# Optimization experiments

Hardware: AMD Instinct MI355X
Metric: run time of the kernel (lower is better)

The kernel has to match this reference:

```python
import jax, jax.numpy as jnp
import numpy as np

HEADS = 8
DIM_HEAD = 64
SCALE = DIM_HEAD ** -0.5


def setup_inputs() -> dict:
    key = jax.random.key(0)
    ks = jax.random.split(key, 5)
    B, N, D = 2, 4096, 512
    x = jax.random.normal(ks[0], (B, N, D), dtype=jnp.float32)
    Wq = jax.random.normal(ks[1], (D, D), dtype=jnp.float32) * (D ** -0.5)
    Wk = jax.random.normal(ks[2], (D, D), dtype=jnp.float32) * (D ** -0.5)
    Wv = jax.random.normal(ks[3], (D, D), dtype=jnp.float32) * (D ** -0.5)
    Wo = jax.random.normal(ks[4], (D, D), dtype=jnp.float32) * (D ** -0.5)
    bo = jnp.zeros((D,), dtype=jnp.float32)
    return {"x": x, "Wq": Wq, "Wk": Wk, "Wv": Wv, "Wo": Wo, "bo": bo}


def reference(x, Wq, Wk, Wv, Wo, bo):
    B, N, D = x.shape
    h, d = HEADS, DIM_HEAD
    # torch nn.Linear: y = x @ W.T
    q = (x @ Wq.T).reshape(B, N, h, d).transpose(0, 2, 1, 3)  # b h n d
    k = (x @ Wk.T).reshape(B, N, h, d).transpose(0, 2, 1, 3)
    v = (x @ Wv.T).reshape(B, N, h, d).transpose(0, 2, 1, 3)
    # fp32 score path (ATTN_PRECISION='fp32')
    sim = jnp.einsum('bhid,bhjd->bhij', q.astype(jnp.float32), k.astype(jnp.float32)) * SCALE
    attn = jax.nn.softmax(sim, axis=-1).astype(v.dtype)
    out = jnp.einsum('bhij,bhjd->bhid', attn, v)  # b h n d
    out = out.transpose(0, 2, 1, 3).reshape(B, N, h * d)  # b n (h d)
    return out @ Wo.T + bo
```

## Files before the change

kernel.cpp:

```cpp
#include <hip/hip_runtime.h>
#include <hip/hip_bf16.h>

#define B_ 2
#define N_ 4096
#define D_ 512
#define H_ 8
#define M_ (B_*N_)
#define QSCALE_ 0.18033688011f

typedef short bf16x8 __attribute__((ext_vector_type(8)));
typedef float f32x4  __attribute__((ext_vector_type(4)));

static __device__ __forceinline__ unsigned short f2bf(float f) {
    union { float f; unsigned int u; } v; v.f = f;
    unsigned int r = v.u + 0x7fffu + ((v.u >> 16) & 1u);
    return (unsigned short)(r >> 16);
}
static __device__ __forceinline__ float bf2f(unsigned short h) {
    union { unsigned int u; float f; } v; v.u = ((unsigned int)h) << 16;
    return v.f;
}
static __device__ __forceinline__ unsigned int cvt_pk_bf16(float a, float b) {
    unsigned int r;
    asm("v_cvt_pk_bf16_f32 %0, %1, %2" : "=v"(r) : "v"(a), "v"(b));
    return r;
}

__global__ void conv_all(const float* __restrict__ x,
                         const float* __restrict__ w0, const float* __restrict__ w1,
                         const float* __restrict__ w2, const float* __restrict__ w3,
                         unsigned short* __restrict__ xh, unsigned short* __restrict__ xl,
                         unsigned short* __restrict__ wh, unsigned short* __restrict__ wl)
{
    const int i = blockIdx.x * 256 + threadIdx.x;
    float4 v;
    ushort4* dh;
    ushort4* dl;
    if (i < 1048576) {
        v = ((const float4*)x)[i];
        dh = (ushort4*)xh + i;
        dl = (ushort4*)xl + i;
    } else {
        const int j = i - 1048576;
        const int w = j >> 16, di = j & 65535;
        const float* src = w == 0 ? w0 : w == 1 ? w1 : w == 2 ? w2 : w3;
        v = ((const float4*)src)[di];
        dh = (ushort4*)(wh + (size_t)w * 262144) + di;
        dl = (ushort4*)(wl + (size_t)w * 262144) + di;
    }
    ushort4 hv, lv;
    hv.x = f2bf(v.x); hv.y = f2bf(v.y); hv.z = f2bf(v.z); hv.w = f2bf(v.w);
    lv.x = f2bf(v.x - bf2f(hv.x)); lv.y = f2bf(v.y - bf2f(hv.y));
    lv.z = f2bf(v.z - bf2f(hv.z)); lv.w = f2bf(v.w - bf2f(hv.w));
    *dh = hv;
    *dl = lv;
}

template<int MODE>
__global__ __launch_bounds__(256, 2) void gemm_mfma(
    const unsigned short* __restrict__ Ah, const unsigned short* __restrict__ Al,
    const unsigned short* __restrict__ Wh, const unsigned short* __restrict__ Wl,
    const float* __restrict__ bias, float* __restrict__ outF,
    unsigned short* __restrict__ oh0, unsigned short* __restrict__ ol0,
    unsigned short* __restrict__ oh1, unsigned short* __restrict__ ol1,
    unsigned short* __restrict__ oh2, unsigned short* __restrict__ ol2,
    float scale0)
{
    __shared__ unsigned short At[2][8192];
    __shared__ unsigned short Bt[2][8192];

    const int t = threadIdx.x;
    const int lane = t & 63, wave = t >> 6;
    const int l15 = lane & 15, g = lane >> 4;
    const int wr = wave >> 1, wc = wave & 1;
    const int mb = blockIdx.x * 128;

    int which = 0, nbeff;
    if (MODE == 1) { which = blockIdx.y >> 2; nbeff = (blockIdx.y & 3) * 128; }
    else           { nbeff = blockIdx.y * 128; }
    const unsigned short* Whp = Wh + (size_t)which * 262144;
    const unsigned short* Wlp = Wl + (size_t)which * 262144;

    const int srow = t >> 1, sh = t & 1;
    const size_t gAr = (size_t)(mb + srow) * 512 + sh * 16;
    const size_t gBr = (size_t)(nbeff + srow) * 512 + sh * 16;
    const int sw = srow & 7;
    const int dA0 = srow * 64 + (((sh * 2 + 0) ^ sw) * 8);
    const int dA1 = srow * 64 + (((sh * 2 + 1) ^ sw) * 8);
    const int dA2 = srow * 64 + (((sh * 2 + 4) ^ sw) * 8);
    const int dA3 = srow * 64 + (((sh * 2 + 5) ^ sw) * 8);

    bf16x8 sA[4], sB[4];
#define GLOAD(K0) do {                                                              \
        sA[0] = *(const bf16x8*)&Ah[gAr + (K0)];  sA[1] = *(const bf16x8*)&Ah[gAr + (K0) + 8];  \
        sA[2] = *(const bf16x8*)&Al[gAr + (K0)];  sA[3] = *(const bf16x8*)&Al[gAr + (K0) + 8];  \
        sB[0] = *(const bf16x8*)&Whp[gBr + (K0)]; sB[1] = *(const bf16x8*)&Whp[gBr + (K0) + 8]; \
        sB[2] = *(const bf16x8*)&Wlp[gBr + (K0)]; sB[3] = *(const bf16x8*)&Wlp[gBr + (K0) + 8]; \
    } while (0)
#define SWRITE(BB) do {                                                             \
        *(bf16x8*)&At[BB][dA0] = sA[0]; *(bf16x8*)&At[BB][dA1] = sA[1];             \
        *(bf16x8*)&At[BB][dA2] = sA[2]; *(bf16x8*)&At[BB][dA3] = sA[3];             \
        *(bf16x8*)&Bt[BB][dA0] = sB[0]; *(bf16x8*)&Bt[BB][dA1] = sB[1];             \
        *(bf16x8*)&Bt[BB][dA2] = sB[2]; *(bf16x8*)&Bt[BB][dA3] = sB[3];             \
    } while (0)

    f32x4 acc[4][4];
#pragma unroll
    for (int mi = 0; mi < 4; ++mi)
#pragma unroll
        for (int ni = 0; ni < 4; ++ni) acc[mi][ni] = (f32x4){0.f, 0.f, 0.f, 0.f};

    GLOAD(0); SWRITE(0); __syncthreads();
    int cur = 0;
    for (int ks = 0; ks < 16; ++ks) {
        if (ks < 15) GLOAD((ks + 1) * 32);

        bf16x8 afh[4], afl[4], wfh[4], wfl[4];
#pragma unroll
        for (int mi = 0; mi < 4; ++mi) {
            const int ar = wr * 64 + mi * 16 + l15, asw = ar & 7;
            afh[mi] = *(const bf16x8*)&At[cur][ar * 64 + ((g ^ asw) * 8)];
            afl[mi] = *(const bf16x8*)&At[cur][ar * 64 + (((g + 4) ^ asw) * 8)];
        }
#pragma unroll
        for (int ni = 0; ni < 4; ++ni) {
            const int br = wc * 64 + ni * 16 + l15, bsw = br & 7;
            wfh[ni] = *(const bf16x8*)&Bt[cur][br * 64 + ((g ^ bsw) * 8)];
            wfl[ni] = *(const bf16x8*)&Bt[cur][br * 64 + (((g + 4) ^ bsw) * 8)];
        }
#pragma unroll
        for (int mi = 0; mi < 4; ++mi)
#pragma unroll
            for (int ni = 0; ni < 4; ++ni) {
                acc[mi][ni] = __builtin_amdgcn_mfma_f32_16x16x32_bf16(afh[mi], wfh[ni], acc[mi][ni], 0, 0, 0);
                acc[mi][ni] = __builtin_amdgcn_mfma_f32_16x16x32_bf16(afl[mi], wfh[ni], acc[mi][ni], 0, 0, 0);
                acc[mi][ni] = __builtin_amdgcn_mfma_f32_16x16x32_bf16(afh[mi], wfl[ni], acc[mi][ni], 0, 0, 0);
            }

        if (ks < 15) SWRITE(cur ^ 1);
        __syncthreads();
        cur ^= 1;
    }
#undef GLOAD
#undef SWRITE

    if (MODE == 0) {
#pragma unroll
        for (int ni = 0; ni < 4; ++ni) {
            const int col = nbeff + wc * 64 + ni * 16 + l15;
            const float bv = bias[col];
#pragma unroll
            for (int mi = 0; mi < 4; ++mi) {
                const int m0 = mb + wr * 64 + mi * 16 + g * 4;
#pragma unroll
                for (int r = 0; r < 4; ++r)
                    outF[(size_t)(m0 + r) * 512 + col] = acc[mi][ni][r] + bv;
            }
        }
    } else if (which < 2) {
        unsigned short* oh = which ? oh1 : oh0;
        unsigned short* ol = which ? ol1 : ol0;
        const float scl = which ? 1.0f : scale0;
#pragma unroll
        for (int ni = 0; ni < 4; ++ni) {
            const int col = nbeff + wc * 64 + ni * 16 + l15;
            const int hh = col >> 6, dd = col & 63;
#pragma unroll
            for (int mi = 0; mi < 4; ++mi) {
                const int m0 = mb + wr * 64 + mi * 16 + g * 4;
                const int b = m0 >> 12, seq0 = m0 & (N_ - 1);
                const size_t base = ((size_t)(b * H_ + hh) * N_ + seq0) * 64 + dd;
#pragma unroll
                for (int r = 0; r < 4; ++r) {
                    const float s = acc[mi][ni][r] * scl;
                    const unsigned short hv = f2bf(s);
                    oh[base + (size_t)r * 64] = hv;
                    ol[base + (size_t)r * 64] = f2bf(s - bf2f(hv));
                }
            }
        }
    } else {
#pragma unroll
        for (int ni = 0; ni < 4; ++ni) {
            const int col = nbeff + wc * 64 + ni * 16 + l15;
            const int hh = col >> 6, dd = col & 63;
#pragma unroll
            for (int mi = 0; mi < 4; ++mi) {
                const int m0 = mb + wr * 64 + mi * 16 + g * 4;
                const int b = m0 >> 12, seq0 = m0 & (N_ - 1);
                const size_t base = ((size_t)((b * H_ + hh) * 64) + dd) * N_ + seq0;
                ushort4 hv;
                hv.x = f2bf(acc[mi][ni][0]); hv.y = f2bf(acc[mi][ni][1]);
                hv.z = f2bf(acc[mi][ni][2]); hv.w = f2bf(acc[mi][ni][3]);
                *(ushort4*)&oh2[base] = hv;
            }
        }
    }
}

__global__ __launch_bounds__(256, 2) void attn_mfma(
    const unsigned short* __restrict__ qh, const unsigned short* __restrict__ ql,
    const unsigned short* __restrict__ kh, const unsigned short* __restrict__ kl,
    const unsigned short* __restrict__ vth,
    unsigned short* __restrict__ oh, unsigned short* __restrict__ ol)
{
    __shared__ unsigned short Kb[2][2][4096];
    __shared__ unsigned short Vb[2][4096];

    const int t    = threadIdx.x;
    const int lane = t & 63;
    const int wave = t >> 6;
    const int l15  = lane & 15;
    const int g    = lane >> 4;
    const int bh   = blockIdx.y;
    const int qbase = blockIdx.x * 128 + wave * 32;

    bf16x8 qf[2][2][2];
#pragma unroll
    for (int rt = 0; rt < 2; ++rt)
#pragma unroll
        for (int c = 0; c < 2; ++c) {
            const size_t src = ((size_t)bh * N_ + qbase + rt * 16 + l15) * 64 + c * 32 + g * 8;
            qf[rt][c][0] = *(const bf16x8*)&qh[src];
            qf[rt][c][1] = *(const bf16x8*)&ql[src];
        }

    f32x4 O[2][4];
#pragma unroll
    for (int rt = 0; rt < 2; ++rt)
#pragma unroll
        for (int dt = 0; dt < 4; ++dt) O[rt][dt] = (f32x4){0.f, 0.f, 0.f, 0.f};
    float mreg[2] = {-3.0e38f, -3.0e38f};
    float lreg[2] = {0.f, 0.f};

    const int srow = t >> 3;
    const int sc16 = t & 7;
    const size_t kbase = (size_t)bh * N_ * 64;
    const size_t vbase = (size_t)bh * 64 * N_;
    const int vdst0 = srow * 64 + ((sc16 ^ (srow & 7)) * 8);
    const int vdst1 = (srow + 32) * 64 + ((sc16 ^ ((srow + 32) & 7)) * 8);
    const int krho  = (((srow >> 2) & 1) << 4) | (((srow >> 3) & 3) << 2) | (srow & 3);
    const int kdst0 = krho * 64 + ((sc16 ^ (krho & 7)) * 8);
    const int kdst1 = kdst0 + 32 * 64;

    bf16x8 sKh[2], sKl[2], sVh[2];

#define LOADT(KT) do {                                                                \
        const size_t gK0 = kbase + ((size_t)((KT) * 64 + srow)) * 64 + sc16 * 8;      \
        const size_t gK1 = kbase + ((size_t)((KT) * 64 + srow + 32)) * 64 + sc16 * 8; \
        const size_t gV0 = vbase + (size_t)srow * N_ + (KT) * 64 + sc16 * 8;          \
        const size_t gV1 = vbase + (size_t)(srow + 32) * N_ + (KT) * 64 + sc16 * 8;   \
        sKh[0] = *(const bf16x8*)&kh[gK0];  sKh[1] = *(const bf16x8*)&kh[gK1];        \
        sKl[0] = *(const bf16x8*)&kl[gK0];  sKl[1] = *(const bf16x8*)&kl[gK1];        \
        sVh[0] = *(const bf16x8*)&vth[gV0]; sVh[1] = *(const bf16x8*)&vth[gV1];       \
    } while (0)

#define WRITET(BB) do {                                                               \
        *(bf16x8*)&Kb[BB][0][kdst0] = sKh[0]; *(bf16x8*)&Kb[BB][0][kdst1] = sKh[1];   \
        *(bf16x8*)&Kb[BB][1][kdst0] = sKl[0]; *(bf16x8*)&Kb[BB][1][kdst1] = sKl[1];   \
        *(bf16x8*)&Vb[BB][vdst0] = sVh[0];    *(bf16x8*)&Vb[BB][vdst1] = sVh[1];      \
    } while (0)

#define QKT_J(J, BUF, S) do {                                                         \
        const int krow_ = (J) * 16 + l15;                                             \
        const int rb_ = krow_ * 64, sw_ = (krow_ & 7) * 8;                            \
        _Pragma("unroll")                                                             \
        for (int c = 0; c < 2; ++c) {                                                 \
            const int off_ = rb_ + (((c * 4 + g) * 8) ^ sw_);                         \
            bf16x8 kfh_ = *(const bf16x8*)&Kb[BUF][0][off_];                          \
            bf16x8 kfl_ = *(const bf16x8*)&Kb[BUF][1][off_];                          \
            _Pragma("unroll")                                                         \
            for (int rt = 0; rt < 2; ++rt) {                                          \
                S[rt][J] = __builtin_amdgcn_mfma_f32_16x16x32_bf16(kfh_, qf[rt][c][0], S[rt][J], 0, 0, 0); \
                S[rt][J] = __builtin_amdgcn_mfma_f32_16x16x32_bf16(kfl_, qf[rt][c][0], S[rt][J], 0, 0, 0); \
                S[rt][J] = __builtin_amdgcn_mfma_f32_16x16x32_bf16(kfh_, qf[rt][c][1], S[rt][J], 0, 0, 0); \
            }                                                                         \
        }                                                                             \
    } while (0)

#define SOFTMAX_RT(RT, S) do {                                                        \
        float pmax_ = -3.0e38f;                                                       \
        _Pragma("unroll")                                                             \
        for (int j = 0; j < 4; ++j)                                                   \
            _Pragma("unroll")                                                         \
            for (int r = 0; r < 4; ++r) pmax_ = fmaxf(pmax_, S[RT][j][r]);            \
        pmax_ = fmaxf(pmax_, __shfl_xor(pmax_, 16));                                  \
        pmax_ = fmaxf(pmax_, __shfl_xor(pmax_, 32));                                  \
        const float mold_ = mreg[RT];                                                 \
        if (!__all(pmax_ <= mold_ + 8.0f)) {                                          \
            const float mnew_ = fmaxf(mold_, pmax_);                                  \
            const float alpha_ = exp2f(mold_ - mnew_);                                \
            _Pragma("unroll")                                                         \
            for (int dt = 0; dt < 4; ++dt)                                            \
                _Pragma("unroll")                                                     \
                for (int r = 0; r < 4; ++r) O[RT][dt][r] *= alpha_;                   \
            lreg[RT] *= alpha_;                                                       \
            mreg[RT] = mnew_;                                                         \
        }                                                                             \
        const float mb_ = mreg[RT];                                                   \
        float lsum_ = 0.f;                                                            \
        _Pragma("unroll")                                                             \
        for (int j = 0; j < 4; ++j)                                                   \
            _Pragma("unroll")                                                         \
            for (int r = 0; r < 4; ++r) {                                             \
                S[RT][j][r] = exp2f(S[RT][j][r] - mb_);                               \
                lsum_ += S[RT][j][r];                                                 \
            }                                                                         \
        lreg[RT] += lsum_;                                                            \
        _Pragma("unroll")                                                             \
        for (int c = 0; c < 2; ++c) {                                                 \
            union { unsigned int u[4]; bf16x8 v; } th_;                               \
            th_.u[0] = cvt_pk_bf16(S[RT][2*c][0], S[RT][2*c][1]);                     \
            th_.u[1] = cvt_pk_bf16(S[RT][2*c][2], S[RT][2*c][3]);                     \
            th_.u[2] = cvt_pk_bf16(S[RT][2*c+1][0], S[RT][2*c+1][1]);                 \
            th_.u[3] = cvt_pk_bf16(S[RT][2*c+1][2], S[RT][2*c+1][3]);                 \
            pah[RT][c] = th_.v;                                                       \
        }                                                                             \
    } while (0)

#define PVSTEP(BUF) do {                                                              \
        _Pragma("unroll")                                                             \
        for (int c = 0; c < 2; ++c)                                                   \
            _Pragma("unroll")                                                         \
            for (int dt = 0; dt < 4; ++dt) {                                          \
                const int vrow_ = dt * 16 + l15;                                      \
                const int off_ = vrow_ * 64 + (((c * 4 + g) * 8) ^ ((vrow_ & 7) * 8));\
                bf16x8 vfh_ = *(const bf16x8*)&Vb[BUF][off_];                         \
                _Pragma("unroll")                                                     \
                for (int rt = 0; rt < 2; ++rt)                                        \
                    O[rt][dt] = __builtin_amdgcn_mfma_f32_16x16x32_bf16(vfh_, pah[rt][c], O[rt][dt], 0, 0, 0); \
            }                                                                         \
    } while (0)

#define ITER(T, BK, SC, SP) do {                                                      \
        if ((T) < 63) LOADT((T) + 1);                                                 \
        __builtin_amdgcn_s_setprio(1);                                                \
        SC[0][0] = (f32x4){0.f,0.f,0.f,0.f}; SC[0][1] = (f32x4){0.f,0.f,0.f,0.f};     \
        SC[0][2] = (f32x4){0.f,0.f,0.f,0.f}; SC[0][3] = (f32x4){0.f,0.f,0.f,0.f};     \
        SC[1][0] = (f32x4){0.f,0.f,0.f,0.f}; SC[1][1] = (f32x4){0.f,0.f,0.f,0.f};     \
        SC[1][2] = (f32x4){0.f,0.f,0.f,0.f}; SC[1][3] = (f32x4){0.f,0.f,0.f,0.f};     \
        QKT_J(0, BK, SC); QKT_J(1, BK, SC);                                           \
        SOFTMAX_RT(0, SP);                                                            \
        QKT_J(2, BK, SC); QKT_J(3, BK, SC);                                           \
        SOFTMAX_RT(1, SP);                                                            \
        PVSTEP((BK) ^ 1);                                                             \
        __builtin_amdgcn_s_setprio(0);                                                \
        __syncthreads();                                                              \
        if ((T) < 63) WRITET((BK) ^ 1);                                               \
        __syncthreads();                                                              \
    } while (0)

    f32x4 Sa[2][4], Sb[2][4];
    bf16x8 pah[2][2];

    LOADT(0); WRITET(0); __syncthreads();
    LOADT(1);
#pragma unroll
    for (int rt = 0; rt < 2; ++rt)
#pragma unroll
        for (int j = 0; j < 4; ++j) Sa[rt][j] = (f32x4){0.f, 0.f, 0.f, 0.f};
    __builtin_amdgcn_s_setprio(1);
    QKT_J(0, 0, Sa); QKT_J(1, 0, Sa); QKT_J(2, 0, Sa); QKT_J(3, 0, Sa);
    __builtin_amdgcn_s_setprio(0);
    WRITET(1);
    __syncthreads();

    for (int tt = 1; tt < 64; tt += 2) {
        ITER(tt, 1, Sb, Sa);
        if (tt + 1 < 64) ITER(tt + 1, 0, Sa, Sb);
    }
    SOFTMAX_RT(0, Sb);
    SOFTMAX_RT(1, Sb);
    PVSTEP(1);

    const int b = bh >> 3, hh = bh & 7;
#pragma unroll
    for (int rt = 0; rt < 2; ++rt) {
        float lt = lreg[rt];
        lt += __shfl_xor(lt, 16);
        lt += __shfl_xor(lt, 32);
        const float inv = 1.0f / lt;
        const int n = qbase + rt * 16 + l15;
        const size_t rowbase = ((size_t)(b * N_) + n) * 512 + hh * 64 + g * 4;
#pragma unroll
        for (int dt = 0; dt < 4; ++dt) {
            const float s0 = O[rt][dt][0] * inv, s1 = O[rt][dt][1] * inv,
                        s2 = O[rt][dt][2] * inv, s3 = O[rt][dt][3] * inv;
            ushort4 hv, lv;
            hv.x = f2bf(s0); hv.y = f2bf(s1); hv.z = f2bf(s2); hv.w = f2bf(s3);
            lv.x = f2bf(s0 - bf2f(hv.x)); lv.y = f2bf(s1 - bf2f(hv.y));
            lv.z = f2bf(s2 - bf2f(hv.z)); lv.w = f2bf(s3 - bf2f(hv.w));
            *(ushort4*)&oh[rowbase + dt * 16] = hv;
            *(ushort4*)&ol[rowbase + dt * 16] = lv;
        }
    }
#undef LOADT
#undef WRITET
#undef QKT_J
#undef SOFTMAX_RT
#undef PVSTEP
#undef ITER
}

extern "C" void kernel_launch(void* const* d_in, const int* in_sizes, int n_in,
                              void* d_out, int out_size, void* d_ws, size_t ws_size,
                              hipStream_t stream)
{
    const float* x  = (const float*)d_in[0];
    const float* Wq = (const float*)d_in[1];
    const float* Wk = (const float*)d_in[2];
    const float* Wv = (const float*)d_in[3];
    const float* Wo = (const float*)d_in[4];
    const float* bo = (const float*)d_in[5];

    unsigned char* w8 = (unsigned char*)d_ws;
    const size_t MB = 1024 * 1024;
    unsigned short* xh  = (unsigned short*)(w8);
    unsigned short* xl  = (unsigned short*)(w8 + 8  * MB);
    unsigned short* wh  = (unsigned short*)(w8 + 16 * MB);
    unsigned short* wl  = (unsigned short*)(w8 + 18 * MB);
    unsigned short* qh  = (unsigned short*)(w8 + 20 * MB);
    unsigned short* ql  = (unsigned short*)(w8 + 28 * MB);
    unsigned short* kh  = (unsigned short*)(w8 + 36 * MB);
    unsigned short* kl  = (unsigned short*)(w8 + 44 * MB);
    unsigned short* vth = (unsigned short*)(w8 + 52 * MB);
    unsigned short* ah = xh;
    unsigned short* al = xl;
    float* out = (float*)d_out;

    conv_all<<<5120, 256, 0, stream>>>(x, Wq, Wk, Wv, Wo, xh, xl, wh, wl);

    gemm_mfma<1><<<dim3(64, 12), 256, 0, stream>>>(xh, xl, wh, wl, nullptr, nullptr,
                                                   qh, ql, kh, kl, vth, nullptr, QSCALE_);

    attn_mfma<<<dim3(N_ / 128, 16), 256, 0, stream>>>(qh, ql, kh, kl, vth, ah, al);

    gemm_mfma<0><<<dim3(64, 4), 256, 0, stream>>>(ah, al, wh + 3 * 262144, wl + 3 * 262144,
                                                  bo, out, nullptr, nullptr, nullptr, nullptr,
                                                  nullptr, nullptr, 1.0f);
}
```

Before: 304.8 us.

## Use 8 waves of 16 query rows per attention block instead of 4x32

The attention kernel now launches 512 threads per block, with each wave owning 16 query rows instead of 32. This halves per-wave accumulator, Q-fragment and score registers, so launch bounds can target more waves per SIMD. The K/V tile load is split across twice as many threads, so each thread loads one chunk instead of two. In exchange, each K/V fragment read from LDS feeds half as many MFMAs, which raises LDS traffic relative to compute, and the larger block makes each barrier cost more.

```diff
diff --git a/kernel.cpp b/kernel.cpp
--- a/kernel.cpp
+++ b/kernel.cpp
@@ -198,7 +198,7 @@
     }
 }
 
-__global__ __launch_bounds__(256, 2) void attn_mfma(
+__global__ __launch_bounds__(512, 4) void attn_mfma(
     const unsigned short* __restrict__ qh, const unsigned short* __restrict__ ql,
     const unsigned short* __restrict__ kh, const unsigned short* __restrict__ kl,
     const unsigned short* __restrict__ vth,
@@ -213,52 +213,44 @@
     const int l15  = lane & 15;
     const int g    = lane >> 4;
     const int bh   = blockIdx.y;
-    const int qbase = blockIdx.x * 128 + wave * 32;
-
-    bf16x8 qf[2][2][2];
-#pragma unroll
-    for (int rt = 0; rt < 2; ++rt)
-#pragma unroll
-        for (int c = 0; c < 2; ++c) {
-            const size_t src = ((size_t)bh * N_ + qbase + rt * 16 + l15) * 64 + c * 32 + g * 8;
-            qf[rt][c][0] = *(const bf16x8*)&qh[src];
-            qf[rt][c][1] = *(const bf16x8*)&ql[src];
-        }
-
-    f32x4 O[2][4];
-#pragma unroll
-    for (int rt = 0; rt < 2; ++rt)
-#pragma unroll
-        for (int dt = 0; dt < 4; ++dt) O[rt][dt] = (f32x4){0.f, 0.f, 0.f, 0.f};
-    float mreg[2] = {-3.0e38f, -3.0e38f};
-    float lreg[2] = {0.f, 0.f};
+    const int qbase = blockIdx.x * 128 + wave * 16;
+
+    bf16x8 qf[2][2];
+#pragma unroll
+    for (int c = 0; c < 2; ++c) {
+        const size_t src = ((size_t)bh * N_ + qbase + l15) * 64 + c * 32 + g * 8;
+        qf[c][0] = *(const bf16x8*)&qh[src];
+        qf[c][1] = *(const bf16x8*)&ql[src];
+    }
+
+    f32x4 O[4];
+#pragma unroll
+    for (int dt = 0; dt < 4; ++dt) O[dt] = (f32x4){0.f, 0.f, 0.f, 0.f};
+    float mreg = -3.0e38f, lreg = 0.f;
 
     const int srow = t >> 3;
     const int sc16 = t & 7;
     const size_t kbase = (size_t)bh * N_ * 64;
     const size_t vbase = (size_t)bh * 64 * N_;
-    const int vdst0 = srow * 64 + ((sc16 ^ (srow & 7)) * 8);
-    const int vdst1 = (srow + 32) * 64 + ((sc16 ^ ((srow + 32) & 7)) * 8);
-    const int krho  = (((srow >> 2) & 1) << 4) | (((srow >> 3) & 3) << 2) | (srow & 3);
-    const int kdst0 = krho * 64 + ((sc16 ^ (krho & 7)) * 8);
-    const int kdst1 = kdst0 + 32 * 64;
-
-    bf16x8 sKh[2], sKl[2], sVh[2];
+    const int vdst = srow * 64 + ((sc16 ^ (srow & 7)) * 8);
+    const int krho = ((srow >> 5) << 5) | (((srow >> 2) & 1) << 4)
+                   | (((srow >> 3) & 3) << 2) | (srow & 3);
+    const int kdst = krho * 64 + ((sc16 ^ (krho & 7)) * 8);
+
+    bf16x8 sKh, sKl, sVh;
 
 #define LOADT(KT) do {                                                                \
-        const size_t gK0 = kbase + ((size_t)((KT) * 64 + srow)) * 64 + sc16 * 8;      \
-        const size_t gK1 = kbase + ((size_t)((KT) * 64 + srow + 32)) * 64 + sc16 * 8; \
-        const size_t gV0 = vbase + (size_t)srow * N_ + (KT) * 64 + sc16 * 8;          \
-        const size_t gV1 = vbase + (size_t)(srow + 32) * N_ + (KT) * 64 + sc16 * 8;   \
-        sKh[0] = *(const bf16x8*)&kh[gK0];  sKh[1] = *(const bf16x8*)&kh[gK1];        \
-        sKl[0] = *(const bf16x8*)&kl[gK0];  sKl[1] = *(const bf16x8*)&kl[gK1];        \
-        sVh[0] = *(const bf16x8*)&vth[gV0]; sVh[1] = *(const bf16x8*)&vth[gV1];       \
+        const size_t gK = kbase + ((size_t)((KT) * 64 + srow)) * 64 + sc16 * 8;       \
+        const size_t gV = vbase + (size_t)srow * N_ + (KT) * 64 + sc16 * 8;           \
+        sKh = *(const bf16x8*)&kh[gK];                                                \
+        sKl = *(const bf16x8*)&kl[gK];                                                \
+        sVh = *(const bf16x8*)&vth[gV];                                               \
     } while (0)
 
 #define WRITET(BB) do {                                                               \
-        *(bf16x8*)&Kb[BB][0][kdst0] = sKh[0]; *(bf16x8*)&Kb[BB][0][kdst1] = sKh[1];   \
-        *(bf16x8*)&Kb[BB][1][kdst0] = sKl[0]; *(bf16x8*)&Kb[BB][1][kdst1] = sKl[1];   \
-        *(bf16x8*)&Vb[BB][vdst0] = sVh[0];    *(bf16x8*)&Vb[BB][vdst1] = sVh[1];      \
+        *(bf16x8*)&Kb[BB][0][kdst] = sKh;                                             \
+        *(bf16x8*)&Kb[BB][1][kdst] = sKl;                                             \
+        *(bf16x8*)&Vb[BB][vdst] = sVh;                                                \
     } while (0)
 
 #define QKT_J(J, BUF, S) do {                                                         \
@@ -269,52 +261,49 @@
             const int off_ = rb_ + (((c * 4 + g) * 8) ^ sw_);                         \
             bf16x8 kfh_ = *(const bf16x8*)&Kb[BUF][0][off_];                          \
             bf16x8 kfl_ = *(const bf16x8*)&Kb[BUF][1][off_];                          \
-            _Pragma("unroll")                                                         \
-            for (int rt = 0; rt < 2; ++rt) {                                          \
-                S[rt][J] = __builtin_amdgcn_mfma_f32_16x16x32_bf16(kfh_, qf[rt][c][0], S[rt][J], 0, 0, 0); \
-                S[rt][J] = __builtin_amdgcn_mfma_f32_16x16x32_bf16(kfl_, qf[rt][c][0], S[rt][J], 0, 0, 0); \
-                S[rt][J] = __builtin_amdgcn_mfma_f32_16x16x32_bf16(kfh_, qf[rt][c][1], S[rt][J], 0, 0, 0); \
-            }                                                                         \
+            S[J] = __builtin_amdgcn_mfma_f32_16x16x32_bf16(kfh_, qf[c][0], S[J], 0, 0, 0); \
+            S[J] = __builtin_amdgcn_mfma_f32_16x16x32_bf16(kfl_, qf[c][0], S[J], 0, 0, 0); \
+            S[J] = __builtin_amdgcn_mfma_f32_16x16x32_bf16(kfh_, qf[c][1], S[J], 0, 0, 0); \
         }                                                                             \
     } while (0)
 
-#define SOFTMAX_RT(RT, S) do {                                                        \
+#define SOFTMAX_T(S) do {                                                             \
         float pmax_ = -3.0e38f;                                                       \
         _Pragma("unroll")                                                             \
         for (int j = 0; j < 4; ++j)                                                   \
             _Pragma("unroll")                                                         \
-            for (int r = 0; r < 4; ++r) pmax_ = fmaxf(pmax_, S[RT][j][r]);            \
+            for (int r = 0; r < 4; ++r) pmax_ = fmaxf(pmax_, S[j][r]);                \
         pmax_ = fmaxf(pmax_, __shfl_xor(pmax_, 16));                                  \
         pmax_ = fmaxf(pmax_, __shfl_xor(pmax_, 32));                                  \
-        const float mold_ = mreg[RT];                                                 \
+        const float mold_ = mreg;                                                     \
         if (!__all(pmax_ <= mold_ + 8.0f)) {                                          \
             const float mnew_ = fmaxf(mold_, pmax_);                                  \
             const float alpha_ = exp2f(mold_ - mnew_);                                \
             _Pragma("unroll")                                                         \
             for (int dt = 0; dt < 4; ++dt)                                            \
                 _Pragma("unroll")                                                     \
-                for (int r = 0; r < 4; ++r) O[RT][dt][r] *= alpha_;                   \
-            lreg[RT] *= alpha_;                                                       \
-            mreg[RT] = mnew_;                                                         \
+                for (int r = 0; r < 4; ++r) O[dt][r] *= alpha_;                       \
+            lreg *= alpha_;                                                           \
+            mreg = mnew_;                                                             \
         }                                                                             \
-        const float mb_ = mreg[RT];                                                   \
+        const float mb_ = mreg;                                                       \
         float lsum_ = 0.f;                                                            \
         _Pragma("unroll")                                                             \
         for (int j = 0; j < 4; ++j)                                                   \
             _Pragma("unroll")                                                         \
             for (int r = 0; r < 4; ++r) {                                             \
-                S[RT][j][r] = exp2f(S[RT][j][r] - mb_);                               \
-                lsum_ += S[RT][j][r];                                                 \
+                S[j][r] = exp2f(S[j][r] - mb_);                                       \
+                lsum_ += S[j][r];                                                     \
             }                                                                         \
-        lreg[RT] += lsum_;                                                            \
+        lreg += lsum_;                                                                \
         _Pragma("unroll")                                                             \
         for (int c = 0; c < 2; ++c) {                                                 \
             union { unsigned int u[4]; bf16x8 v; } th_;                               \
-            th_.u[0] = cvt_pk_bf16(S[RT][2*c][0], S[RT][2*c][1]);                     \
-            th_.u[1] = cvt_pk_bf16(S[RT][2*c][2], S[RT][2*c][3]);                     \
-            th_.u[2] = cvt_pk_bf16(S[RT][2*c+1][0], S[RT][2*c+1][1]);                 \
-            th_.u[3] = cvt_pk_bf16(S[RT][2*c+1][2], S[RT][2*c+1][3]);                 \
-            pah[RT][c] = th_.v;                                                       \
+            th_.u[0] = cvt_pk_bf16(S[2*c][0], S[2*c][1]);                             \
+            th_.u[1] = cvt_pk_bf16(S[2*c][2], S[2*c][3]);                             \
+            th_.u[2] = cvt_pk_bf16(S[2*c+1][0], S[2*c+1][1]);                         \
+            th_.u[3] = cvt_pk_bf16(S[2*c+1][2], S[2*c+1][3]);                         \
+            pah[c] = th_.v;                                                           \
         }                                                                             \
     } while (0)
 
@@ -326,23 +315,18 @@
                 const int vrow_ = dt * 16 + l15;                                      \
                 const int off_ = vrow_ * 64 + (((c * 4 + g) * 8) ^ ((vrow_ & 7) * 8));\
                 bf16x8 vfh_ = *(const bf16x8*)&Vb[BUF][off_];                         \
-                _Pragma("unroll")                                                     \
-                for (int rt = 0; rt < 2; ++rt)                                        \
-                    O[rt][dt] = __builtin_amdgcn_mfma_f32_16x16x32_bf16(vfh_, pah[rt][c], O[rt][dt], 0, 0, 0); \
+                O[dt] = __builtin_amdgcn_mfma_f32_16x16x32_bf16(vfh_, pah[c], O[dt], 0, 0, 0); \
             }                                                                         \
     } while (0)
 
 #define ITER(T, BK, SC, SP) do {                                                      \
         if ((T) < 63) LOADT((T) + 1);                                                 \
         __builtin_amdgcn_s_setprio(1);                                                \
-        SC[0][0] = (f32x4){0.f,0.f,0.f,0.f}; SC[0][1] = (f32x4){0.f,0.f,0.f,0.f};     \
-        SC[0][2] = (f32x4){0.f,0.f,0.f,0.f}; SC[0][3] = (f32x4){0.f,0.f,0.f,0.f};     \
-        SC[1][0] = (f32x4){0.f,0.f,0.f,0.f}; SC[1][1] = (f32x4){0.f,0.f,0.f,0.f};     \
-        SC[1][2] = (f32x4){0.f,0.f,0.f,0.f}; SC[1][3] = (f32x4){0.f,0.f,0.f,0.f};     \
+        SC[0] = (f32x4){0.f,0.f,0.f,0.f}; SC[1] = (f32x4){0.f,0.f,0.f,0.f};           \
+        SC[2] = (f32x4){0.f,0.f,0.f,0.f}; SC[3] = (f32x4){0.f,0.f,0.f,0.f};           \
         QKT_J(0, BK, SC); QKT_J(1, BK, SC);                                           \
-        SOFTMAX_RT(0, SP);                                                            \
+        SOFTMAX_T(SP);                                                                \
         QKT_J(2, BK, SC); QKT_J(3, BK, SC);                                           \
-        SOFTMAX_RT(1, SP);                                                            \
         PVSTEP((BK) ^ 1);                                                             \
         __builtin_amdgcn_s_setprio(0);                                                \
         __syncthreads();                                                              \
@@ -350,15 +334,13 @@
         __syncthreads();                                                              \
     } while (0)
 
-    f32x4 Sa[2][4], Sb[2][4];
-    bf16x8 pah[2][2];
+    f32x4 Sa[4], Sb[4];
+    bf16x8 pah[2];
 
     LOADT(0); WRITET(0); __syncthreads();
     LOADT(1);
 #pragma unroll
-    for (int rt = 0; rt < 2; ++rt)
-#pragma unroll
-        for (int j = 0; j < 4; ++j) Sa[rt][j] = (f32x4){0.f, 0.f, 0.f, 0.f};
+    for (int j = 0; j < 4; ++j) Sa[j] = (f32x4){0.f, 0.f, 0.f, 0.f};
     __builtin_amdgcn_s_setprio(1);
     QKT_J(0, 0, Sa); QKT_J(1, 0, Sa); QKT_J(2, 0, Sa); QKT_J(3, 0, Sa);
     __builtin_amdgcn_s_setprio(0);
@@ -369,23 +351,21 @@
         ITER(tt, 1, Sb, Sa);
         if (tt + 1 < 64) ITER(tt + 1, 0, Sa, Sb);
     }
-    SOFTMAX_RT(0, Sb);
-    SOFTMAX_RT(1, Sb);
+    SOFTMAX_T(Sb);
     PVSTEP(1);
 
     const int b = bh >> 3, hh = bh & 7;
-#pragma unroll
-    for (int rt = 0; rt < 2; ++rt) {
-        float lt = lreg[rt];
+    {
+        float lt = lreg;
         lt += __shfl_xor(lt, 16);
         lt += __shfl_xor(lt, 32);
         const float inv = 1.0f / lt;
-        const int n = qbase + rt * 16 + l15;
+        const int n = qbase + l15;
         const size_t rowbase = ((size_t)(b * N_) + n) * 512 + hh * 64 + g * 4;
 #pragma unroll
         for (int dt = 0; dt < 4; ++dt) {
-            const float s0 = O[rt][dt][0] * inv, s1 = O[rt][dt][1] * inv,
-                        s2 = O[rt][dt][2] * inv, s3 = O[rt][dt][3] * inv;
+            const float s0 = O[dt][0] * inv, s1 = O[dt][1] * inv,
+                        s2 = O[dt][2] * inv, s3 = O[dt][3] * inv;
             ushort4 hv, lv;
             hv.x = f2bf(s0); hv.y = f2bf(s1); hv.z = f2bf(s2); hv.w = f2bf(s3);
             lv.x = f2bf(s0 - bf2f(hv.x)); lv.y = f2bf(s1 - bf2f(hv.y));
@@ -397,7 +377,7 @@
 #undef LOADT
 #undef WRITET
 #undef QKT_J
-#undef SOFTMAX_RT
+#undef SOFTMAX_T
 #undef PVSTEP
 #undef ITER
 }
@@ -433,7 +413,7 @@
     gemm_mfma<1><<<dim3(64, 12), 256, 0, stream>>>(xh, xl, wh, wl, nullptr, nullptr,
                                                    qh, ql, kh, kl, vth, nullptr, QSCALE_);
 
-    attn_mfma<<<dim3(N_ / 128, 16), 256, 0, stream>>>(qh, ql, kh, kl, vth, ah, al);
+    attn_mfma<<<dim3(N_ / 128, 16), 512, 0, stream>>>(qh, ql, kh, kl, vth, ah, al);
 
     gemm_mfma<0><<<dim3(64, 4), 256, 0, stream>>>(ah, al, wh + 3 * 262144, wl + 3 * 262144,
                                                   bo, out, nullptr, nullptr, nullptr, nullptr,
```

Measured after the change: 304.2 us. No clear change (-0.2%).
